# Kernel optimization log

Hardware: AMD Instinct MI355X
Metric: run time of the kernel (lower is better)

The kernel has to match this reference:

```python
import jax, jax.numpy as jnp
import numpy as np

D_MODEL = 512
NHEAD = 8
HEAD_DIM = D_MODEL // NHEAD
LN_EPS = 1e-5


def layer_norm(x, gamma, beta):
    mu = jnp.mean(x, axis=-1, keepdims=True)
    var = jnp.var(x, axis=-1, keepdims=True)
    return (x - mu) * jax.lax.rsqrt(var + LN_EPS) * gamma + beta


def setup_inputs() -> dict:
    key = jax.random.key(0)
    ks = jax.random.split(key, 10)
    B, L, S = 2, 4096, 4096
    d = D_MODEL
    s = 0.02
    return {
        "x": jax.random.normal(ks[0], (B, L, d), dtype=jnp.float32),
        "source": jax.random.normal(ks[1], (B, S, d), dtype=jnp.float32),
        "Wq": jax.random.normal(ks[2], (d, d), dtype=jnp.float32) * s,
        "Wk": jax.random.normal(ks[3], (d, d), dtype=jnp.float32) * s,
        "Wv": jax.random.normal(ks[4], (d, d), dtype=jnp.float32) * s,
        "Wm": jax.random.normal(ks[5], (d, d), dtype=jnp.float32) * s,
        "W1": jax.random.normal(ks[6], (2 * d, 2 * d), dtype=jnp.float32) * s,
        "W2": jax.random.normal(ks[7], (d, 2 * d), dtype=jnp.float32) * s,
        "g1": jnp.ones((d,), dtype=jnp.float32),
        "b1": jnp.zeros((d,), dtype=jnp.float32),
        "g2": jnp.ones((d,), dtype=jnp.float32),
        "b2": jnp.zeros((d,), dtype=jnp.float32),
    }


def reference(x, source, Wq, Wk, Wv, Wm, W1, W2, g1, b1, g2, b2):
    bs, L, _ = x.shape
    S = source.shape[1]
    # projections (torch Linear: y = x @ W^T), split into heads
    qw = (x @ Wq.T).reshape(bs, L, NHEAD, HEAD_DIM)
    kw = (source @ Wk.T).reshape(bs, S, NHEAD, HEAD_DIM)
    vw = (source @ Wv.T).reshape(bs, S, NHEAD, HEAD_DIM)
    # attention scores [B, L, S, H], softmax over S (axis=2)
    a = jnp.einsum('nlhd,nshd->nlsh', qw, kw) / jnp.sqrt(jnp.float32(HEAD_DIM))
    a = jax.nn.softmax(a, axis=2)
    o = jnp.einsum('nlsh,nshd->nlhd', a, vw).reshape(bs, L, NHEAD * HEAD_DIM)
    message = layer_norm(o @ Wm.T, g1, b1)
    h = jnp.concatenate([x, message], axis=2)  # [B, L, 2D]
    h = jax.nn.relu(h @ W1.T) @ W2.T
    message = layer_norm(h, g2, b2)
    return x + message
```

## Files before the change

kernel.cpp:

```cpp
#include <hip/hip_runtime.h>
#include <stdint.h>

typedef short bh8 __attribute__((ext_vector_type(8)));
typedef float fx4 __attribute__((ext_vector_type(4)));
typedef float fx16 __attribute__((ext_vector_type(16)));
typedef unsigned short u16;
typedef unsigned int u32;
typedef u32 u32x4 __attribute__((ext_vector_type(4)));
typedef u16 us4 __attribute__((ext_vector_type(4)));

#define NHEAD 8
#define HD 64
#define DM 512
#define SEQ 4096
#define ROWS 8192
#define CEXP 0.1803368801111244f

#define MODE_F32 0
#define MODE_BF16 1
#define MODE_RELU_BF16 2
#define MODE_KV 3

__device__ __forceinline__ u16 f2bf(float f) {
  union { float f; u32 u; } x; x.f = f;
  u32 u = x.u;
  u = u + 0x7fffu + ((u >> 16) & 1u);
  return (u16)(u >> 16);
}
__device__ __forceinline__ float bf2f(u16 h) {
  union { u32 u; float f; } x; x.u = ((u32)h) << 16;
  return x.f;
}
__device__ __forceinline__ void gll16(const void* g, void* l) {
  __builtin_amdgcn_global_load_lds(
      (const __attribute__((address_space(1))) void*)(uintptr_t)g,
      (__attribute__((address_space(3))) void*)(uintptr_t)l,
      16, 0, 0);
}
__device__ __forceinline__ fx4 mfma16(bh8 a, bh8 b, fx4 c) {
  return __builtin_amdgcn_mfma_f32_16x16x32_bf16(a, b, c, 0, 0, 0);
}
__device__ __forceinline__ fx16 mfma32(bh8 a, bh8 b, fx16 c) {
  return __builtin_amdgcn_mfma_f32_32x32x16_bf16(a, b, c, 0, 0, 0);
}
__device__ __forceinline__ u32 cvtpk(float lo, float hi) {
  u32 r; asm("v_cvt_pk_bf16_f32 %0, %1, %2" : "=v"(r) : "v"(lo), "v"(hi));
  return r;
}
__device__ __forceinline__ void pswap(u32& a, u32& b) {
  auto r = __builtin_amdgcn_permlane32_swap(a, b, false, false);
  a = r[0]; b = r[1];
}

__global__ __launch_bounds__(256) void cvt2_kernel(const float* __restrict__ a,
                                                   const float* __restrict__ b,
                                                   u16* __restrict__ da,
                                                   u16* __restrict__ db) {
  const int nq = ROWS * DM / 4;
  for (int i = blockIdx.x * 256 + threadIdx.x; i < 2 * nq; i += gridDim.x * 256) {
    const float* s; u16* d; int j;
    if (i < nq) { s = a; d = da; j = i; } else { s = b; d = db; j = i - nq; }
    float4 v = ((const float4*)s)[j];
    us4 o; o.x = f2bf(v.x); o.y = f2bf(v.y); o.z = f2bf(v.z); o.w = f2bf(v.w);
    ((us4*)d)[j] = o;
  }
}

__global__ __launch_bounds__(256) void cvtw_kernel(
    const float* __restrict__ Wq, const float* __restrict__ Wk,
    const float* __restrict__ Wv, const float* __restrict__ Wm,
    const float* __restrict__ W1, const float* __restrict__ W2,
    u16* __restrict__ wqb, u16* __restrict__ wkvb, u16* __restrict__ wmb,
    u16* __restrict__ w1b, u16* __restrict__ w2b) {
  for (int i = blockIdx.x * 256 + threadIdx.x; i < 655360; i += gridDim.x * 256) {
    const float* s; u16* d; int j;
    if (i < 65536)       { s = Wq; d = wqb;            j = i; }
    else if (i < 131072) { s = Wk; d = wkvb;           j = i - 65536; }
    else if (i < 196608) { s = Wv; d = wkvb + 262144;  j = i - 131072; }
    else if (i < 262144) { s = Wm; d = wmb;            j = i - 196608; }
    else if (i < 524288) { s = W1; d = w1b;            j = i - 262144; }
    else                 { s = W2; d = w2b;            j = i - 524288; }
    float4 v = ((const float4*)s)[j];
    us4 o; o.x = f2bf(v.x); o.y = f2bf(v.y); o.z = f2bf(v.z); o.w = f2bf(v.w);
    ((us4*)d)[j] = o;
  }
}

__global__ __launch_bounds__(256) void gemm_bt_kernel(
    const u16* __restrict__ A, const u16* __restrict__ Bw,
    void* __restrict__ Cp, void* __restrict__ C2p,
    int M, int N, int K, int mode) {
  __shared__ __attribute__((aligned(16))) char smem[2 * 128 * 128];
  char* sA = smem;
  char* sB = smem + 128 * 128;
  const int tid = threadIdx.x;
  const int w = tid >> 6, l = tid & 63;
  const int fr = l & 15, fg = l >> 4;
  const int row0 = blockIdx.y * 128, col0 = blockIdx.x * 128;
  const int wr = (w >> 1) * 64, wc = (w & 1) * 64;

  fx4 acc[4][4];
#pragma unroll
  for (int m = 0; m < 4; m++)
#pragma unroll
    for (int n = 0; n < 4; n++)
#pragma unroll
      for (int r = 0; r < 4; r++) acc[m][n][r] = 0.f;

  for (int k0 = 0; k0 < K; k0 += 64) {
    __syncthreads();
#pragma unroll
    for (int i = 0; i < 4; i++) {
      int t = i * 256 + tid;
      int r = t >> 3, g = t & 7;
      int gs = g ^ (r & 7);
      gll16(A + (size_t)(row0 + r) * K + k0 + gs * 8, sA + i * 4096 + w * 1024);
      gll16(Bw + (size_t)(col0 + r) * K + k0 + gs * 8, sB + i * 4096 + w * 1024);
    }
    __syncthreads();
#pragma unroll
    for (int ks = 0; ks < 2; ks++) {
      bh8 af[4], bfr[4];
#pragma unroll
      for (int m = 0; m < 4; m++) {
        int rr = wr + m * 16 + fr;
        af[m] = *(const bh8*)(sA + rr * 128 + ((ks * 64 + fg * 16) ^ ((rr & 7) << 4)));
      }
#pragma unroll
      for (int n = 0; n < 4; n++) {
        int rr = wc + n * 16 + fr;
        bfr[n] = *(const bh8*)(sB + rr * 128 + ((ks * 64 + fg * 16) ^ ((rr & 7) << 4)));
      }
#pragma unroll
      for (int m = 0; m < 4; m++)
#pragma unroll
        for (int n = 0; n < 4; n++) acc[m][n] = mfma16(af[m], bfr[n], acc[m][n]);
    }
  }
#pragma unroll
  for (int m = 0; m < 4; m++)
#pragma unroll
    for (int n = 0; n < 4; n++)
#pragma unroll
      for (int r = 0; r < 4; r++) {
        int row = row0 + wr + m * 16 + fg * 4 + r;
        int col = col0 + wc + n * 16 + fr;
        float v = acc[m][n][r];
        if (mode == MODE_F32) {
          ((float*)Cp)[(size_t)row * N + col] = v;
        } else if (mode == MODE_BF16) {
          ((u16*)Cp)[(size_t)row * N + col] = f2bf(v);
        } else if (mode == MODE_RELU_BF16) {
          ((u16*)Cp)[(size_t)row * N + col] = f2bf(v > 0.f ? v : 0.f);
        } else {
          if (col < 512) {
            ((u16*)Cp)[(size_t)row * 512 + col] = f2bf(v);
          } else {
            int dd = col - 512;
            int bb = row >> 12, s = row & 4095;
            ((u16*)C2p)[((size_t)(bb * NHEAD + (dd >> 6)) * HD + (dd & 63)) * SEQ + s] = f2bf(v);
          }
        }
      }
}

__global__ __launch_bounds__(256) void gemm64_kernel(
    const u16* __restrict__ A, const u16* __restrict__ Bw,
    void* __restrict__ Cp, int M, int N, int K, int mode) {
  __shared__ __attribute__((aligned(16))) char smem[128 * 128 + 64 * 128];
  char* sA = smem;
  char* sB = smem + 128 * 128;
  const int tid = threadIdx.x;
  const int w = tid >> 6, l = tid & 63;
  const int fr = l & 15, fg = l >> 4;
  const int row0 = blockIdx.y * 128, col0 = blockIdx.x * 64;
  const int wr = (w >> 1) * 64, wc = (w & 1) * 32;

  fx4 acc[4][2];
#pragma unroll
  for (int m = 0; m < 4; m++)
#pragma unroll
    for (int n = 0; n < 2; n++)
#pragma unroll
      for (int r = 0; r < 4; r++) acc[m][n][r] = 0.f;

  for (int k0 = 0; k0 < K; k0 += 64) {
    __syncthreads();
#pragma unroll
    for (int i = 0; i < 4; i++) {
      int t = i * 256 + tid;
      int r = t >> 3, g = t & 7;
      int gs = g ^ (r & 7);
      gll16(A + (size_t)(row0 + r) * K + k0 + gs * 8, sA + i * 4096 + w * 1024);
    }
#pragma unroll
    for (int i = 0; i < 2; i++) {
      int t = i * 256 + tid;
      int r = t >> 3, g = t & 7;
      int gs = g ^ (r & 7);
      gll16(Bw + (size_t)(col0 + r) * K + k0 + gs * 8, sB + i * 4096 + w * 1024);
    }
    __syncthreads();
#pragma unroll
    for (int ks = 0; ks < 2; ks++) {
      bh8 af[4], bfr[2];
#pragma unroll
      for (int m = 0; m < 4; m++) {
        int rr = wr + m * 16 + fr;
        af[m] = *(const bh8*)(sA + rr * 128 + ((ks * 64 + fg * 16) ^ ((rr & 7) << 4)));
      }
#pragma unroll
      for (int n = 0; n < 2; n++) {
        int rr = wc + n * 16 + fr;
        bfr[n] = *(const bh8*)(sB + rr * 128 + ((ks * 64 + fg * 16) ^ ((rr & 7) << 4)));
      }
#pragma unroll
      for (int m = 0; m < 4; m++)
#pragma unroll
        for (int n = 0; n < 2; n++) acc[m][n] = mfma16(af[m], bfr[n], acc[m][n]);
    }
  }
#pragma unroll
  for (int m = 0; m < 4; m++)
#pragma unroll
    for (int n = 0; n < 2; n++)
#pragma unroll
      for (int r = 0; r < 4; r++) {
        int row = row0 + wr + m * 16 + fg * 4 + r;
        int col = col0 + wc + n * 16 + fr;
        float v = acc[m][n][r];
        if (mode == MODE_F32) ((float*)Cp)[(size_t)row * N + col] = v;
        else                  ((u16*)Cp)[(size_t)row * N + col] = f2bf(v);
      }
}

__global__ __launch_bounds__(256, 4) void attn_kernel(
    const u16* __restrict__ Q, const u16* __restrict__ Kb,
    const u16* __restrict__ Vt, u16* __restrict__ Op0, u16* __restrict__ Op1,
    float* __restrict__ lsum) {
  __shared__ __attribute__((aligned(16))) char sm[2][2][8192];
  const int tid = threadIdx.x;
  const int w = tid >> 6, l = tid & 63;
  const int l31 = l & 31, hi = l >> 5;
  const int swz = (l31 & 7) << 4;

  int dl = blockIdx.y * gridDim.x + blockIdx.x;
  int bh = ((dl & 7) << 1) | ((dl >> 3) & 1);
  int rest = dl >> 4;
  int bx = rest & 31, half = rest >> 5;
  const int b = bh >> 3, h = bh & 7;
  const int qr0 = b * SEQ + bx * 128 + w * 32;
  const int sbase = half * (SEQ / 2);

  auto STAGE = [&](int buf, int t) {
    int s0 = sbase + t * 64;
#pragma unroll
    for (int i = 0; i < 2; i++) {
      int gl = i * 256 + tid;
      int r = gl >> 3, g = gl & 7;
      int gs = g ^ (r & 7);
      gll16(Kb + (size_t)(b * SEQ + s0 + r) * DM + h * HD + gs * 8,
            &sm[buf][0][0] + i * 4096 + w * 1024);
      gll16(Vt + (size_t)(bh * HD + r) * SEQ + s0 + gs * 8,
            &sm[buf][1][0] + i * 4096 + w * 1024);
    }
  };

  STAGE(0, 0);

  bh8 qf[4];
#pragma unroll
  for (int ks = 0; ks < 4; ks++)
    qf[ks] = *(const bh8*)(Q + (size_t)(qr0 + l31) * DM + h * HD + ks * 16 + hi * 8);

  fx16 o0, o1;
#pragma unroll
  for (int r = 0; r < 16; r++) { o0[r] = 0.f; o1[r] = 0.f; }
  float l_run = 0.f;

  __syncthreads();

  const int NT = SEQ / 2 / 64;
  for (int t = 0; t < NT; ++t) {
    int cur = t & 1;
    if (t < NT - 1) STAGE(cur ^ 1, t + 1);
    const char* sK = &sm[cur][0][0];
    const char* sV = &sm[cur][1][0];

    fx16 s0v, s1v;
#pragma unroll
    for (int r = 0; r < 16; r++) { s0v[r] = 0.f; s1v[r] = 0.f; }
    __builtin_amdgcn_s_setprio(1);
#pragma unroll
    for (int ks = 0; ks < 4; ks++) {
      int off = (ks * 32 + hi * 16) ^ swz;
      bh8 k0 = *(const bh8*)(sK + l31 * 128 + off);
      bh8 k1 = *(const bh8*)(sK + (l31 + 32) * 128 + off);
      s0v = mfma32(k0, qf[ks], s0v);
      s1v = mfma32(k1, qf[ks], s1v);
    }
    __builtin_amdgcn_s_setprio(0);

    float rs = 0.f;
#pragma unroll
    for (int r = 0; r < 16; r++) {
      s0v[r] = __builtin_amdgcn_exp2f(s0v[r] * CEXP); rs += s0v[r];
    }
#pragma unroll
    for (int r = 0; r < 16; r++) {
      s1v[r] = __builtin_amdgcn_exp2f(s1v[r] * CEXP); rs += s1v[r];
    }
    l_run += rs;

    __builtin_amdgcn_s_setprio(1);
#pragma unroll
    for (int ks = 0; ks < 4; ks++) {
      int o8 = (ks & 1) * 8;
      u32 w0a, w1a, w0b, w1b;
      if (ks < 2) {
        w0a = cvtpk(s0v[o8 + 0], s0v[o8 + 1]);
        w1a = cvtpk(s0v[o8 + 2], s0v[o8 + 3]);
        w0b = cvtpk(s0v[o8 + 4], s0v[o8 + 5]);
        w1b = cvtpk(s0v[o8 + 6], s0v[o8 + 7]);
      } else {
        w0a = cvtpk(s1v[o8 + 0], s1v[o8 + 1]);
        w1a = cvtpk(s1v[o8 + 2], s1v[o8 + 3]);
        w0b = cvtpk(s1v[o8 + 4], s1v[o8 + 5]);
        w1b = cvtpk(s1v[o8 + 6], s1v[o8 + 7]);
      }
      pswap(w0a, w0b); pswap(w1a, w1b);
      u32x4 fw; fw.x = w0a; fw.y = w1a; fw.z = w0b; fw.w = w1b;
      bh8 pa = __builtin_bit_cast(bh8, fw);
      int off = (ks * 32 + hi * 16) ^ swz;
      bh8 v0 = *(const bh8*)(sV + l31 * 128 + off);
      bh8 v1 = *(const bh8*)(sV + (l31 + 32) * 128 + off);
      o0 = mfma32(pa, v0, o0);
      o1 = mfma32(pa, v1, o1);
    }
    __builtin_amdgcn_s_setprio(0);
    __syncthreads();
  }

  l_run += __shfl_xor(l_run, 32);
  if (hi == 0)
    lsum[half * 65536 + bh * 4096 + ((qr0 & 4095) + l31)] = l_run;
  u16* Op = half ? Op1 : Op0;
#pragma unroll
  for (int r = 0; r < 16; r++) {
    int crow = (r & 3) + 8 * (r >> 2) + 4 * hi;
    size_t row = (size_t)(qr0 + crow);
    Op[row * DM + h * HD + l31] = f2bf(o0[r]);
    Op[row * DM + h * HD + 32 + l31] = f2bf(o1[r]);
  }
}

__global__ __launch_bounds__(256) void merge_kernel(
    const u16* __restrict__ Oa, const u16* __restrict__ Ob,
    const float* __restrict__ lsum, u16* __restrict__ out) {
  int i8 = blockIdx.x * 256 + threadIdx.x;
  size_t base = (size_t)i8 * 8;
  if (base >= (size_t)ROWS * DM) return;
  int row = (int)(base >> 9), col = (int)(base & 511);
  int h = col >> 6, b = row >> 12, lr = row & 4095;
  float la = lsum[(b * 8 + h) * 4096 + lr];
  float lb = lsum[65536 + (b * 8 + h) * 4096 + lr];
  float inv = 1.f / (la + lb);
  bh8 va = *(const bh8*)(Oa + base);
  bh8 vb = *(const bh8*)(Ob + base);
  bh8 o;
#pragma unroll
  for (int j = 0; j < 8; j++)
    o[j] = (short)f2bf((bf2f((u16)va[j]) + bf2f((u16)vb[j])) * inv);
  *(bh8*)(out + base) = o;
}

__global__ __launch_bounds__(256) void ln_concat_kernel(
    const u16* __restrict__ M0, const u16* __restrict__ xb,
    const float* __restrict__ g1, const float* __restrict__ b1,
    u16* __restrict__ h) {
  const int row = blockIdx.x;
  const int tid = threadIdx.x;
  const u16* mr = M0 + (size_t)row * 512;
  float v0 = bf2f(mr[tid]), v1 = bf2f(mr[tid + 256]);
  float s = v0 + v1, s2 = v0 * v0 + v1 * v1;
#pragma unroll
  for (int off = 1; off <= 32; off <<= 1) {
    s += __shfl_xor(s, off);
    s2 += __shfl_xor(s2, off);
  }
  __shared__ float red[8];
  const int w = tid >> 6, l = tid & 63;
  if (l == 0) { red[w] = s; red[w + 4] = s2; }
  __syncthreads();
  s = red[0] + red[1] + red[2] + red[3];
  s2 = red[4] + red[5] + red[6] + red[7];
  float mu = s * (1.f / 512.f);
  float var = s2 * (1.f / 512.f) - mu * mu;
  float rstd = rsqrtf(var + 1e-5f);
  u16* hr = h + (size_t)row * 1024;
  const u16* xrow = xb + (size_t)row * 512;
  for (int e = tid; e < 512; e += 256) {
    hr[e] = xrow[e];
    hr[512 + e] = f2bf((bf2f(mr[e]) - mu) * rstd * g1[e] + b1[e]);
  }
}

__global__ __launch_bounds__(256) void ln_res_kernel(
    const float* __restrict__ F, const float* __restrict__ X,
    const float* __restrict__ g2, const float* __restrict__ b2,
    float* __restrict__ out) {
  const int row = blockIdx.x;
  const int tid = threadIdx.x;
  const float* fr_ = F + (size_t)row * 512;
  float v0 = fr_[tid], v1 = fr_[tid + 256];
  float s = v0 + v1, s2 = v0 * v0 + v1 * v1;
#pragma unroll
  for (int off = 1; off <= 32; off <<= 1) {
    s += __shfl_xor(s, off);
    s2 += __shfl_xor(s2, off);
  }
  __shared__ float red[8];
  const int w = tid >> 6, l = tid & 63;
  if (l == 0) { red[w] = s; red[w + 4] = s2; }
  __syncthreads();
  s = red[0] + red[1] + red[2] + red[3];
  s2 = red[4] + red[5] + red[6] + red[7];
  float mu = s * (1.f / 512.f);
  float var = s2 * (1.f / 512.f) - mu * mu;
  float rstd = rsqrtf(var + 1e-5f);
  const float* xr = X + (size_t)row * 512;
  float* orow = out + (size_t)row * 512;
  for (int e = tid; e < 512; e += 256)
    orow[e] = xr[e] + (fr_[e] - mu) * rstd * g2[e] + b2[e];
}

extern "C" void kernel_launch(void* const* d_in, const int* in_sizes, int n_in,
                              void* d_out, int out_size, void* d_ws, size_t ws_size,
                              hipStream_t stream) {
  (void)in_sizes; (void)n_in; (void)out_size; (void)ws_size;
  const float* x   = (const float*)d_in[0];
  const float* src = (const float*)d_in[1];
  const float* Wq  = (const float*)d_in[2];
  const float* Wk  = (const float*)d_in[3];
  const float* Wv  = (const float*)d_in[4];
  const float* Wm  = (const float*)d_in[5];
  const float* W1  = (const float*)d_in[6];
  const float* W2  = (const float*)d_in[7];
  const float* g1  = (const float*)d_in[8];
  const float* b1  = (const float*)d_in[9];
  const float* g2  = (const float*)d_in[10];
  const float* b2  = (const float*)d_in[11];

  char* ws = (char*)d_ws;
  u16* xb   = (u16*)(ws + 0);
  u16* sb   = (u16*)(ws + 8388608);
  u16* wqb  = (u16*)(ws + 16777216);
  u16* wkvb = (u16*)(ws + 17301504);
  u16* wmb  = (u16*)(ws + 18350080);
  u16* w1b  = (u16*)(ws + 18874368);
  u16* w2b  = (u16*)(ws + 20971520);
  u16* Qb   = (u16*)(ws + 22020096);
  u16* Kb   = (u16*)(ws + 30408704);
  u16* Vtb  = (u16*)(ws + 38797312);
  u16* Op0  = (u16*)(ws + 47185920);
  u16* Op1  = (u16*)(ws + 8388608);
  float* lsum = (float*)(ws + 55574528);
  u16* Obf  = (u16*)(ws + 22020096);
  u16* M0b  = (u16*)(ws + 30408704);
  u16* hb   = (u16*)(ws + 38797312);
  u16* h1b  = (u16*)(ws + 22020096);
  float* fb = (float*)(ws + 38797312);

  cvt2_kernel<<<2048, 256, 0, stream>>>(x, src, xb, sb);
  cvtw_kernel<<<1024, 256, 0, stream>>>(Wq, Wk, Wv, Wm, W1, W2,
                                        wqb, wkvb, wmb, w1b, w2b);

  gemm64_kernel<<<dim3(8, 64), 256, 0, stream>>>(xb, wqb, Qb, ROWS, 512, 512, MODE_BF16);
  gemm_bt_kernel<<<dim3(8, 64), 256, 0, stream>>>(sb, wkvb, Kb, Vtb, ROWS, 1024, 512, MODE_KV);
  attn_kernel<<<dim3(32, 32), 256, 0, stream>>>(Qb, Kb, Vtb, Op0, Op1, lsum);
  merge_kernel<<<2048, 256, 0, stream>>>(Op0, Op1, lsum, Obf);
  gemm64_kernel<<<dim3(8, 64), 256, 0, stream>>>(Obf, wmb, M0b, ROWS, 512, 512, MODE_BF16);
  ln_concat_kernel<<<8192, 256, 0, stream>>>(M0b, xb, g1, b1, hb);
  gemm_bt_kernel<<<dim3(8, 64), 256, 0, stream>>>(hb, w1b, h1b, nullptr, ROWS, 1024, 1024, MODE_RELU_BF16);
  gemm64_kernel<<<dim3(8, 64), 256, 0, stream>>>(h1b, w2b, fb, ROWS, 512, 1024, MODE_F32);
  ln_res_kernel<<<8192, 256, 0, stream>>>(fb, x, g2, b2, (float*)d_out);
}
```

Baseline: 232.8 us.

## Double query rows per attention wave and fold softmax scale into Q projection

Each attention wave now handles 64 query rows instead of 32, so every K/V tile loaded into shared memory feeds twice as many MFMAs. The grid shrinks to 512 blocks of 256 queries each, and the launch-bounds occupancy hint is dropped. The exp2 scale constant is folded into the Q projection GEMM epilogue, which removes a multiply per score element. The cost is roughly double the accumulator registers, which lowers occupancy. Q is also rounded to bf16 after scaling, which slightly changes numerics.

```diff
diff --git a/kernel.cpp b/kernel.cpp
--- a/kernel.cpp
+++ b/kernel.cpp
@@ -166,7 +166,7 @@
 
 __global__ __launch_bounds__(256) void gemm64_kernel(
     const u16* __restrict__ A, const u16* __restrict__ Bw,
-    void* __restrict__ Cp, int M, int N, int K, int mode) {
+    void* __restrict__ Cp, int M, int N, int K, int mode, float scl) {
   __shared__ __attribute__((aligned(16))) char smem[128 * 128 + 64 * 128];
   char* sA = smem;
   char* sB = smem + 128 * 128;
@@ -230,11 +230,11 @@
         int col = col0 + wc + n * 16 + fr;
         float v = acc[m][n][r];
         if (mode == MODE_F32) ((float*)Cp)[(size_t)row * N + col] = v;
-        else                  ((u16*)Cp)[(size_t)row * N + col] = f2bf(v);
-      }
-}
-
-__global__ __launch_bounds__(256, 4) void attn_kernel(
+        else                  ((u16*)Cp)[(size_t)row * N + col] = f2bf(v * scl);
+      }
+}
+
+__global__ __launch_bounds__(256) void attn_kernel(
     const u16* __restrict__ Q, const u16* __restrict__ Kb,
     const u16* __restrict__ Vt, u16* __restrict__ Op0, u16* __restrict__ Op1,
     float* __restrict__ lsum) {
@@ -244,12 +244,13 @@
   const int l31 = l & 31, hi = l >> 5;
   const int swz = (l31 & 7) << 4;
 
-  int dl = blockIdx.y * gridDim.x + blockIdx.x;
-  int bh = ((dl & 7) << 1) | ((dl >> 3) & 1);
-  int rest = dl >> 4;
-  int bx = rest & 31, half = rest >> 5;
+  int dl = blockIdx.x;
+  int c = dl & 7, j = dl >> 3;
+  int bh = 2 * c + (j >> 5);
+  int rest = j & 31;
+  int qb = rest & 15, half = rest >> 4;
   const int b = bh >> 3, h = bh & 7;
-  const int qr0 = b * SEQ + bx * 128 + w * 32;
+  const int qr0 = b * SEQ + qb * 256 + w * 64;
   const int sbase = half * (SEQ / 2);
 
   auto STAGE = [&](int buf, int t) {
@@ -268,15 +269,17 @@
 
   STAGE(0, 0);
 
-  bh8 qf[4];
-#pragma unroll
-  for (int ks = 0; ks < 4; ks++)
-    qf[ks] = *(const bh8*)(Q + (size_t)(qr0 + l31) * DM + h * HD + ks * 16 + hi * 8);
-
-  fx16 o0, o1;
-#pragma unroll
-  for (int r = 0; r < 16; r++) { o0[r] = 0.f; o1[r] = 0.f; }
-  float l_run = 0.f;
+  bh8 qf0[4], qf1[4];
+#pragma unroll
+  for (int ks = 0; ks < 4; ks++) {
+    qf0[ks] = *(const bh8*)(Q + (size_t)(qr0 + l31) * DM + h * HD + ks * 16 + hi * 8);
+    qf1[ks] = *(const bh8*)(Q + (size_t)(qr0 + 32 + l31) * DM + h * HD + ks * 16 + hi * 8);
+  }
+
+  fx16 o00, o01, o10, o11;
+#pragma unroll
+  for (int r = 0; r < 16; r++) { o00[r] = 0.f; o01[r] = 0.f; o10[r] = 0.f; o11[r] = 0.f; }
+  float lr0 = 0.f, lr1 = 0.f;
 
   __syncthreads();
 
@@ -287,70 +290,84 @@
     const char* sK = &sm[cur][0][0];
     const char* sV = &sm[cur][1][0];
 
-    fx16 s0v, s1v;
-#pragma unroll
-    for (int r = 0; r < 16; r++) { s0v[r] = 0.f; s1v[r] = 0.f; }
+    fx16 s00, s01, s10, s11;
+#pragma unroll
+    for (int r = 0; r < 16; r++) { s00[r] = 0.f; s01[r] = 0.f; s10[r] = 0.f; s11[r] = 0.f; }
     __builtin_amdgcn_s_setprio(1);
 #pragma unroll
     for (int ks = 0; ks < 4; ks++) {
       int off = (ks * 32 + hi * 16) ^ swz;
       bh8 k0 = *(const bh8*)(sK + l31 * 128 + off);
       bh8 k1 = *(const bh8*)(sK + (l31 + 32) * 128 + off);
-      s0v = mfma32(k0, qf[ks], s0v);
-      s1v = mfma32(k1, qf[ks], s1v);
+      s00 = mfma32(k0, qf0[ks], s00);
+      s10 = mfma32(k0, qf1[ks], s10);
+      s01 = mfma32(k1, qf0[ks], s01);
+      s11 = mfma32(k1, qf1[ks], s11);
     }
     __builtin_amdgcn_s_setprio(0);
 
-    float rs = 0.f;
+    float rs0 = 0.f, rs1 = 0.f;
 #pragma unroll
     for (int r = 0; r < 16; r++) {
-      s0v[r] = __builtin_amdgcn_exp2f(s0v[r] * CEXP); rs += s0v[r];
+      s00[r] = __builtin_amdgcn_exp2f(s00[r]); rs0 += s00[r];
+      s10[r] = __builtin_amdgcn_exp2f(s10[r]); rs1 += s10[r];
     }
 #pragma unroll
     for (int r = 0; r < 16; r++) {
-      s1v[r] = __builtin_amdgcn_exp2f(s1v[r] * CEXP); rs += s1v[r];
-    }
-    l_run += rs;
+      s01[r] = __builtin_amdgcn_exp2f(s01[r]); rs0 += s01[r];
+      s11[r] = __builtin_amdgcn_exp2f(s11[r]); rs1 += s11[r];
+    }
+    lr0 += rs0; lr1 += rs1;
 
     __builtin_amdgcn_s_setprio(1);
 #pragma unroll
     for (int ks = 0; ks < 4; ks++) {
       int o8 = (ks & 1) * 8;
-      u32 w0a, w1a, w0b, w1b;
+      u32 a0, a1, b0, b1, c0, c1, d0, d1;
       if (ks < 2) {
-        w0a = cvtpk(s0v[o8 + 0], s0v[o8 + 1]);
-        w1a = cvtpk(s0v[o8 + 2], s0v[o8 + 3]);
-        w0b = cvtpk(s0v[o8 + 4], s0v[o8 + 5]);
-        w1b = cvtpk(s0v[o8 + 6], s0v[o8 + 7]);
+        a0 = cvtpk(s00[o8 + 0], s00[o8 + 1]); a1 = cvtpk(s00[o8 + 2], s00[o8 + 3]);
+        b0 = cvtpk(s00[o8 + 4], s00[o8 + 5]); b1 = cvtpk(s00[o8 + 6], s00[o8 + 7]);
+        c0 = cvtpk(s10[o8 + 0], s10[o8 + 1]); c1 = cvtpk(s10[o8 + 2], s10[o8 + 3]);
+        d0 = cvtpk(s10[o8 + 4], s10[o8 + 5]); d1 = cvtpk(s10[o8 + 6], s10[o8 + 7]);
       } else {
-        w0a = cvtpk(s1v[o8 + 0], s1v[o8 + 1]);
-        w1a = cvtpk(s1v[o8 + 2], s1v[o8 + 3]);
-        w0b = cvtpk(s1v[o8 + 4], s1v[o8 + 5]);
-        w1b = cvtpk(s1v[o8 + 6], s1v[o8 + 7]);
-      }
-      pswap(w0a, w0b); pswap(w1a, w1b);
-      u32x4 fw; fw.x = w0a; fw.y = w1a; fw.z = w0b; fw.w = w1b;
-      bh8 pa = __builtin_bit_cast(bh8, fw);
+        a0 = cvtpk(s01[o8 + 0], s01[o8 + 1]); a1 = cvtpk(s01[o8 + 2], s01[o8 + 3]);
+        b0 = cvtpk(s01[o8 + 4], s01[o8 + 5]); b1 = cvtpk(s01[o8 + 6], s01[o8 + 7]);
+        c0 = cvtpk(s11[o8 + 0], s11[o8 + 1]); c1 = cvtpk(s11[o8 + 2], s11[o8 + 3]);
+        d0 = cvtpk(s11[o8 + 4], s11[o8 + 5]); d1 = cvtpk(s11[o8 + 6], s11[o8 + 7]);
+      }
+      pswap(a0, b0); pswap(a1, b1); pswap(c0, d0); pswap(c1, d1);
+      u32x4 f0; f0.x = a0; f0.y = a1; f0.z = b0; f0.w = b1;
+      u32x4 f1; f1.x = c0; f1.y = c1; f1.z = d0; f1.w = d1;
+      bh8 pa0 = __builtin_bit_cast(bh8, f0);
+      bh8 pa1 = __builtin_bit_cast(bh8, f1);
       int off = (ks * 32 + hi * 16) ^ swz;
       bh8 v0 = *(const bh8*)(sV + l31 * 128 + off);
       bh8 v1 = *(const bh8*)(sV + (l31 + 32) * 128 + off);
-      o0 = mfma32(pa, v0, o0);
-      o1 = mfma32(pa, v1, o1);
+      o00 = mfma32(pa0, v0, o00);
+      o01 = mfma32(pa0, v1, o01);
+      o10 = mfma32(pa1, v0, o10);
+      o11 = mfma32(pa1, v1, o11);
     }
     __builtin_amdgcn_s_setprio(0);
     __syncthreads();
   }
 
-  l_run += __shfl_xor(l_run, 32);
-  if (hi == 0)
-    lsum[half * 65536 + bh * 4096 + ((qr0 & 4095) + l31)] = l_run;
+  lr0 += __shfl_xor(lr0, 32);
+  lr1 += __shfl_xor(lr1, 32);
+  if (hi == 0) {
+    lsum[half * 65536 + bh * 4096 + ((qr0 & 4095) + l31)] = lr0;
+    lsum[half * 65536 + bh * 4096 + ((qr0 & 4095) + 32 + l31)] = lr1;
+  }
   u16* Op = half ? Op1 : Op0;
 #pragma unroll
   for (int r = 0; r < 16; r++) {
     int crow = (r & 3) + 8 * (r >> 2) + 4 * hi;
-    size_t row = (size_t)(qr0 + crow);
-    Op[row * DM + h * HD + l31] = f2bf(o0[r]);
-    Op[row * DM + h * HD + 32 + l31] = f2bf(o1[r]);
+    size_t row0 = (size_t)(qr0 + crow);
+    size_t row1 = (size_t)(qr0 + 32 + crow);
+    Op[row0 * DM + h * HD + l31] = f2bf(o00[r]);
+    Op[row0 * DM + h * HD + 32 + l31] = f2bf(o01[r]);
+    Op[row1 * DM + h * HD + l31] = f2bf(o10[r]);
+    Op[row1 * DM + h * HD + 32 + l31] = f2bf(o11[r]);
   }
 }
 
@@ -475,13 +492,13 @@
   cvtw_kernel<<<1024, 256, 0, stream>>>(Wq, Wk, Wv, Wm, W1, W2,
                                         wqb, wkvb, wmb, w1b, w2b);
 
-  gemm64_kernel<<<dim3(8, 64), 256, 0, stream>>>(xb, wqb, Qb, ROWS, 512, 512, MODE_BF16);
+  gemm64_kernel<<<dim3(8, 64), 256, 0, stream>>>(xb, wqb, Qb, ROWS, 512, 512, MODE_BF16, CEXP);
   gemm_bt_kernel<<<dim3(8, 64), 256, 0, stream>>>(sb, wkvb, Kb, Vtb, ROWS, 1024, 512, MODE_KV);
-  attn_kernel<<<dim3(32, 32), 256, 0, stream>>>(Qb, Kb, Vtb, Op0, Op1, lsum);
+  attn_kernel<<<512, 256, 0, stream>>>(Qb, Kb, Vtb, Op0, Op1, lsum);
   merge_kernel<<<2048, 256, 0, stream>>>(Op0, Op1, lsum, Obf);
-  gemm64_kernel<<<dim3(8, 64), 256, 0, stream>>>(Obf, wmb, M0b, ROWS, 512, 512, MODE_BF16);
+  gemm64_kernel<<<dim3(8, 64), 256, 0, stream>>>(Obf, wmb, M0b, ROWS, 512, 512, MODE_BF16, 1.0f);
   ln_concat_kernel<<<8192, 256, 0, stream>>>(M0b, xb, g1, b1, hb);
   gemm_bt_kernel<<<dim3(8, 64), 256, 0, stream>>>(hb, w1b, h1b, nullptr, ROWS, 1024, 1024, MODE_RELU_BF16);
-  gemm64_kernel<<<dim3(8, 64), 256, 0, stream>>>(h1b, w2b, fb, ROWS, 512, 1024, MODE_F32);
+  gemm64_kernel<<<dim3(8, 64), 256, 0, stream>>>(h1b, w2b, fb, ROWS, 512, 1024, MODE_F32, 1.0f);
   ln_res_kernel<<<8192, 256, 0, stream>>>(fb, x, g2, b2, (float*)d_out);
 }
```

Measured after the change: 245.9 us. 1.06x slower.
